# Optimization experiments

Hardware: AMD Instinct MI355X
Metric: run time of the kernel (lower is better)

Reference implementation:

```python
import jax, jax.numpy as jnp
import numpy as np

EPS = 1e-5

def conv2d(x, w, stride=1, padding=1, dilation=1):
    # x: [N, C, H, W], w: [O, I, kh, kw]
    return jax.lax.conv_general_dilated(
        x, w, (stride, stride), [(padding, padding), (padding, padding)],
        rhs_dilation=(dilation, dilation),
        dimension_numbers=('NCHW', 'OIHW', 'NCHW'))


def setup_inputs() -> dict:
    key = jax.random.key(0)
    ks = jax.random.split(key, 7)
    T, N, Cin, H, W = 16, 4, 64, 64, 64
    Cout = 64
    x = jax.random.normal(ks[0], (T, N, Cin, H, W), dtype=jnp.float32)
    gamma = jnp.ones((Cin,), jnp.float32)
    beta = jnp.zeros((Cin,), jnp.float32)
    conv1_w = jax.random.normal(ks[1], (3 * Cout, Cin, 3, 3), jnp.float32) * 0.02
    conv1_b = jax.random.normal(ks[2], (3 * Cout,), jnp.float32) * 0.02
    w_h2h = jax.random.normal(ks[3], (3 * Cout, Cout, 3, 3), jnp.float32) * 0.02
    w_c2h = jax.random.normal(ks[4], (3 * Cout, Cout, 3, 3), jnp.float32) * 0.02
    return {"x": x, "gamma": gamma, "beta": beta, "conv1_w": conv1_w,
            "conv1_b": conv1_b, "w_h2h": w_h2h, "w_c2h": w_c2h}


def reference(x, gamma, beta, conv1_w, conv1_b, w_h2h, w_c2h):
    T, N, Cin, H, W = x.shape
    Cout = w_h2h.shape[1]
    # time_to_batch: [T, N, C, H, W] -> [T*N, C, H, W]
    xb = x.reshape(T * N, Cin, H, W)
    # BatchNorm2d (training mode: biased batch stats over N*T, H, W)
    mean = jnp.mean(xb, axis=(0, 2, 3), keepdims=True)
    var = jnp.var(xb, axis=(0, 2, 3), keepdims=True)
    g = gamma.reshape(1, Cin, 1, 1)
    b = beta.reshape(1, Cin, 1, 1)
    bnx = (xb - mean) * jax.lax.rsqrt(var + EPS) * g + b
    # conv1: Cin -> 3*Cout
    y = conv2d(bnx, conv1_w, stride=1, padding=1) + conv1_b.reshape(1, -1, 1, 1)
    # batch_to_time: -> [T, N, 3*Cout, H, W]
    y = y.reshape(T, N, 3 * Cout, H, W)

    # ConvLSTMCell: zero init state is exact (h2h/c2h convs have no bias)
    h0 = jnp.zeros((N, Cout, H, W), y.dtype)
    c0 = jnp.zeros((N, Cout, H, W), y.dtype)

    def step(carry, yt):
        h, c = carry
        tmp = conv2d(c, w_c2h, padding=1) + conv2d(h, w_h2h, padding=1) + yt
        cc_f, cc_o, cc_g = jnp.split(tmp, 3, axis=1)
        f = jax.nn.sigmoid(cc_f)
        o = jax.nn.sigmoid(cc_o)
        gg = jnp.tanh(cc_g)
        c_new = f * c + (1.0 - f) * gg
        h_new = o * jnp.tanh(c_new)
        return (h_new, c_new), h_new

    _, hs = jax.lax.scan(step, (h0, c0), y)
    return hs  # [T, N, Cout, H, W]
```

## Files before the change

kernel.cpp:

```cpp
#include <hip/hip_runtime.h>

typedef unsigned short u16;
typedef unsigned int   u32;
typedef __attribute__((ext_vector_type(8))) short short8;
typedef __attribute__((ext_vector_type(4))) float f32x4;

typedef __attribute__((address_space(1))) const void GASV;
typedef __attribute__((address_space(3))) void LASV;

#define IMG_BYTES  557568
#define WS_SCALE   0
#define WS_SHIFT   256
#define WS_PART    512
#define WS_WA      8704
#define WS_BNXP    672256
#define WS_HC      (WS_BNXP + 64*IMG_BYTES)
#define WS_CSTATE  (WS_HC + 16*IMG_BYTES)

#define SM_IN(j)   ((j)*28512)
#define SM_WB(b)   (85536 + (b)*24576)
#define SMEM_TOT   159264

__device__ __forceinline__ u16 f2b(float f){
  u32 x = __float_as_uint(f);
  return (u16)((x + 0x7fffu + ((x>>16)&1u)) >> 16);
}
__device__ __forceinline__ float sigm(float x){ return 1.f/(1.f+__expf(-x)); }
__device__ __forceinline__ float tanh_(float x){
  float e = __expf(2.f*fabsf(x));
  float t = 1.f - 2.f/(e+1.f);
  return copysignf(t, x);
}

__global__ void k_wt(const float* __restrict__ c1, const float* __restrict__ c2h,
                     const float* __restrict__ h2h, u16* __restrict__ wA){
  int idx = blockIdx.x*256 + threadIdx.x;
  int e = idx & 7;
  int lane = (idx >> 3) & 63;
  int v = idx >> 9;
  int f = v % 12;  v /= 12;
  int cc = v & 1;  v >>= 1;
  int stage = v;
  int j = stage / 9, tap = stage % 9;
  int gate = f >> 2, og = f & 3;
  int och = gate*64 + og*16 + (lane & 15);
  int c = cc*32 + (lane >> 4)*8 + e;
  const float* src = (j==0) ? c1 : ((j==1) ? c2h : h2h);
  wA[idx] = f2b(src[(och*64 + c)*9 + tap]);
}

__global__ void k_bnsum(const float* __restrict__ x, float* __restrict__ part){
  int c = blockIdx.x & 63, g = blockIdx.x >> 6;
  int tid = threadIdx.x, w = tid >> 6, lane = tid & 63;
  float s = 0.f, s2 = 0.f;
  for (int im = 0; im < 4; ++im){
    const float* base = x + (((size_t)((g*4+im)*64 + c)) << 12);
    #pragma unroll
    for (int it = 0; it < 4; ++it){
      float4 v = *(const float4*)(base + (((it<<8) + tid) << 2));
      s  += v.x + v.y + v.z + v.w;
      s2 += v.x*v.x + v.y*v.y + v.z*v.z + v.w*v.w;
    }
  }
  #pragma unroll
  for (int off = 32; off > 0; off >>= 1){
    s  += __shfl_down(s,  off);
    s2 += __shfl_down(s2, off);
  }
  __shared__ float red[8];
  if (lane == 0){ red[w] = s; red[4+w] = s2; }
  __syncthreads();
  if (tid == 0){
    float S  = red[0]+red[1]+red[2]+red[3];
    float S2 = red[4]+red[5]+red[6]+red[7];
    part[(g<<7) + c] = S;
    part[(g<<7) + 64 + c] = S2;
  }
}

__global__ void k_bnfin(const float* __restrict__ part, const float* __restrict__ gamma,
                        const float* __restrict__ beta, float* __restrict__ scale,
                        float* __restrict__ shift){
  int c = threadIdx.x;
  float S = 0.f, S2 = 0.f;
  for (int g = 0; g < 16; ++g){ S += part[(g<<7)+c]; S2 += part[(g<<7)+64+c]; }
  const float inv = 1.f/262144.f;
  float mean = S*inv;
  float var  = S2*inv - mean*mean;
  float sc = gamma[c] * rsqrtf(var + 1e-5f);
  scale[c] = sc;
  shift[c] = beta[c] - mean*sc;
}

__global__ void k_bnx(const float* __restrict__ x, const float* __restrict__ scale,
                      const float* __restrict__ shift, char* __restrict__ bnxp){
  int img = blockIdx.x / 66, rp = blockIdx.x % 66;
  int tid = threadIdx.x;
  char* dstrow = bnxp + (size_t)img*IMG_BYTES + (size_t)rp*8448;
  const uint4 z = {0,0,0,0};
  if (rp == 0 || rp == 65){
    for (int i = tid; i < 528; i += 256) ((uint4*)dstrow)[i] = z;
    return;
  }
  if (tid < 16)
    *(uint4*)(dstrow + (tid>>3)*(65*128) + (tid&7)*16) = z;
  int r = rp - 1;
  int col = tid & 63, cq = tid >> 6;
  const float* xb = x + (((size_t)(img*64 + cq*16)) << 12) + (r<<6) + col;
  union { u16 u[16]; uint4 v[2]; } pk;
  #pragma unroll
  for (int i = 0; i < 16; ++i){
    int c = cq*16 + i;
    float vv = xb[((size_t)i) << 12];
    pk.u[i] = f2b(vv*scale[c] + shift[c]);
  }
  char* dst = dstrow + (size_t)(col + 1)*128 + cq*32;
  *(uint4*)dst = pk.v[0];
  *(uint4*)(dst+16) = pk.v[1];
}

#define STAGE_W(s, b) do {                                                      \
  const char* _gs = wA + (size_t)(s)*24576 + (w*3)*1024 + lane*16;              \
  char* _ls = smem + SM_WB(b) + (w*3)*1024;                                     \
  __builtin_amdgcn_global_load_lds((GASV*)(_gs),        (LASV*)(_ls),        16, 0, 0); \
  __builtin_amdgcn_global_load_lds((GASV*)(_gs + 1024), (LASV*)(_ls + 1024), 16, 0, 0); \
  __builtin_amdgcn_global_load_lds((GASV*)(_gs + 2048), (LASV*)(_ls + 2048), 16, 0, 0); \
} while(0)

__global__ __launch_bounds__(512, 1) void k_step(
    const char* __restrict__ bnxp,
    const char* __restrict__ cpad_s, const char* __restrict__ hpad_s,
    char* __restrict__ cpad_d, char* __restrict__ hpad_d,
    const char* __restrict__ wA, const float* __restrict__ b1,
    float* __restrict__ cstate, float* __restrict__ out, int t)
{
  extern __shared__ __align__(16) char smem[];
  const int tid = threadIdx.x;
  const int w = tid >> 6, lane = tid & 63;
  const int l15 = lane & 15, l4 = lane >> 4;
  const int og = w >> 1, ch = w & 1;
  const int n = blockIdx.x >> 6, row = blockIdx.x & 63;

  const char* gb0 = bnxp   + (size_t)(t*4+n)*IMG_BYTES + row*8448;
  const char* gb1 = cpad_s + (size_t)n*IMG_BYTES + row*8448;
  const char* gb2 = hpad_s + (size_t)n*IMG_BYTES + row*8448;

  f32x4 acc[3][2];
  #pragma unroll
  for (int a = 0; a < 3; ++a)
    #pragma unroll
    for (int b = 0; b < 2; ++b)
      acc[a][b] = (f32x4){0.f,0.f,0.f,0.f};

  STAGE_W(0, 0);
  STAGE_W(1, 1);

  #pragma unroll
  for (int j = 0; j < 3; ++j){
    const char* gbj = (j==0) ? gb0 : ((j==1) ? gb1 : gb2);
    char* dj = smem + SM_IN(j);
    #pragma unroll
    for (int rr = 0; rr < 3; ++rr){
      for (int i = tid; i < 528; i += 512)
        *(uint4*)(dj + rr*9504 + (i>>3)*144 + (i&7)*16) =
            *(const uint4*)(gbj + rr*8448 + i*16);
    }
  }
  __syncthreads();

  #pragma unroll
  for (int j = 0; j < 3; ++j){
    #pragma unroll
    for (int kh = 0; kh < 3; ++kh){
      #pragma unroll
      for (int kw = 0; kw < 3; ++kw){
        const int s = j*9 + kh*3 + kw;
        if (s < 25) STAGE_W(s+2, (s+2)%3);
        {
          const char* ab = smem + SM_WB(s%3) + og*1024 + lane*16;
          const char* ib = smem + SM_IN(j) + kh*9504 + ((ch<<5) + kw + l15)*144 + l4*16;
          #pragma unroll
          for (int cc = 0; cc < 2; ++cc){
            short8 af = *(const short8*)(ab + cc*12288);
            short8 ao = *(const short8*)(ab + cc*12288 + 4096);
            short8 ag = *(const short8*)(ab + cc*12288 + 8192);
            #pragma unroll
            for (int cf = 0; cf < 2; ++cf){
              short8 bf = *(const short8*)(ib + cc*64 + cf*2304);
              acc[0][cf] = __builtin_amdgcn_mfma_f32_16x16x32_bf16(af, bf, acc[0][cf], 0,0,0);
              acc[1][cf] = __builtin_amdgcn_mfma_f32_16x16x32_bf16(ao, bf, acc[1][cf], 0,0,0);
              acc[2][cf] = __builtin_amdgcn_mfma_f32_16x16x32_bf16(ag, bf, acc[2][cf], 0,0,0);
            }
          }
        }
        if (s < 26){
          if (s == 25) asm volatile("s_waitcnt vmcnt(0)" ::: "memory");
          else         asm volatile("s_waitcnt vmcnt(3)" ::: "memory");
          __builtin_amdgcn_s_barrier();
        }
      }
    }
  }

  const size_t cb = ((size_t)(n*64)) << 12;
  const size_t ob = ((size_t)((t*4+n)*64)) << 12;
  const int gc0 = (og << 4) + l4*4;
  char* hrow = hpad_d + (size_t)n*IMG_BYTES + (size_t)(row+1)*8448;
  char* crow = cpad_d + (size_t)n*IMG_BYTES + (size_t)(row+1)*8448;

  #pragma unroll
  for (int cf = 0; cf < 2; ++cf){
    const int col = (ch<<5) + (cf<<4) + l15;
    const int p = (row<<6) + col;
    union { u16 u[4]; uint2 v; } hp, cp2;
    #pragma unroll
    for (int reg = 0; reg < 4; ++reg){
      const int gc = gc0 + reg;
      float fv = acc[0][cf][reg] + b1[gc];
      float ov = acc[1][cf][reg] + b1[64+gc];
      float gv = acc[2][cf][reg] + b1[128+gc];
      float f  = sigm(fv);
      float og_ = sigm(ov);
      float g  = tanh_(gv);
      float* cptr = cstate + cb + (((size_t)gc)<<12) + p;
      float cprev = *cptr;
      float cn = f*cprev + (1.f-f)*g;
      float hn = og_ * tanh_(cn);
      *cptr = cn;
      out[ob + (((size_t)gc)<<12) + p] = hn;
      hp.u[reg]  = f2b(hn);
      cp2.u[reg] = f2b(cn);
    }
    *(uint2*)(hrow + (size_t)(col+1)*128 + gc0*2) = hp.v;
    *(uint2*)(crow + (size_t)(col+1)*128 + gc0*2) = cp2.v;
  }
}

extern "C" void kernel_launch(void* const* d_in, const int* in_sizes, int n_in,
                              void* d_out, int out_size, void* d_ws, size_t ws_size,
                              hipStream_t stream)
{
  (void)in_sizes; (void)n_in; (void)out_size; (void)ws_size;
  const float* x     = (const float*)d_in[0];
  const float* gamma = (const float*)d_in[1];
  const float* beta  = (const float*)d_in[2];
  const float* c1w   = (const float*)d_in[3];
  const float* c1b   = (const float*)d_in[4];
  const float* wh2h  = (const float*)d_in[5];
  const float* wc2h  = (const float*)d_in[6];
  char* ws  = (char*)d_ws;
  float* out = (float*)d_out;

  static int attr_done = 0;
  if (!attr_done){
    hipFuncSetAttribute(reinterpret_cast<const void*>(k_step),
                        hipFuncAttributeMaxDynamicSharedMemorySize, SMEM_TOT);
    attr_done = 1;
  }

  char* hpad0 = ws + WS_HC;
  char* cpad0 = ws + WS_HC + (size_t)4*IMG_BYTES;
  char* hpad1 = ws + WS_HC + (size_t)8*IMG_BYTES;
  char* cpad1 = ws + WS_HC + (size_t)12*IMG_BYTES;

  hipMemsetAsync(ws + WS_HC, 0, (size_t)16*IMG_BYTES, stream);
  hipMemsetAsync(ws + WS_CSTATE, 0, (size_t)4*64*4096*4, stream);

  k_wt<<<1296, 256, 0, stream>>>(c1w, wc2h, wh2h, (u16*)(ws + WS_WA));
  k_bnsum<<<1024, 256, 0, stream>>>(x, (float*)(ws + WS_PART));
  k_bnfin<<<1, 64, 0, stream>>>((const float*)(ws + WS_PART), gamma, beta,
                                (float*)(ws + WS_SCALE), (float*)(ws + WS_SHIFT));
  k_bnx<<<4224, 256, 0, stream>>>(x, (const float*)(ws + WS_SCALE),
                                  (const float*)(ws + WS_SHIFT), ws + WS_BNXP);
  for (int t = 0; t < 16; ++t){
    const char* cs = (t & 1) ? cpad1 : cpad0;
    const char* hs = (t & 1) ? hpad1 : hpad0;
    char* cd = (t & 1) ? cpad0 : cpad1;
    char* hd = (t & 1) ? hpad0 : hpad1;
    k_step<<<256, 512, SMEM_TOT, stream>>>(ws + WS_BNXP, cs, hs, cd, hd,
                                           ws + WS_WA, c1b,
                                           (float*)(ws + WS_CSTATE), out, t);
  }
}
```

Baseline: 389.8 us.

## Split output channels across two blocks and stream input images one at a time

Each step kernel now launches 512 blocks of 256 threads, and each block computes half of the output channel groups. The weight tensor is repacked to match this split. The three input images are no longer all staged up front: they are loaded into a single shared-memory buffer one after another, with a sync before each. Shared memory drops to about 64KB so two blocks can fit per CU. This aims to raise occupancy and spread work over more CUs, at the cost of loading each input row twice and adding barriers.

```diff
diff --git a/kernel.cpp b/kernel.cpp
--- a/kernel.cpp
+++ b/kernel.cpp
@@ -17,10 +17,6 @@
 #define WS_HC      (WS_BNXP + 64*IMG_BYTES)
 #define WS_CSTATE  (WS_HC + 16*IMG_BYTES)
 
-#define SM_IN(j)   ((j)*28512)
-#define SM_WB(b)   (85536 + (b)*24576)
-#define SMEM_TOT   159264
-
 __device__ __forceinline__ u16 f2b(float f){
   u32 x = __float_as_uint(f);
   return (u16)((x + 0x7fffu + ((x>>16)&1u)) >> 16);
@@ -38,12 +34,12 @@
   int e = idx & 7;
   int lane = (idx >> 3) & 63;
   int v = idx >> 9;
-  int f = v % 12;  v /= 12;
-  int cc = v & 1;  v >>= 1;
-  int stage = v;
+  int f2 = v % 12;  v /= 12;
+  int oh = v & 1;
+  int stage = v >> 1;
+  int cc = f2 / 6, gate = (f2 % 6) >> 1, og2 = f2 & 1;
   int j = stage / 9, tap = stage % 9;
-  int gate = f >> 2, og = f & 3;
-  int och = gate*64 + og*16 + (lane & 15);
+  int och = gate*64 + (oh*2 + og2)*16 + (lane & 15);
   int c = cc*32 + (lane >> 4)*8 + e;
   const float* src = (j==0) ? c1 : ((j==1) ? c2h : h2h);
   wA[idx] = f2b(src[(och*64 + c)*9 + tap]);
@@ -119,27 +115,39 @@
   *(uint4*)(dst+16) = pk.v[1];
 }
 
+#define SM_RING(b) (28512 + (b)*12288)
+
 #define STAGE_W(s, b) do {                                                      \
-  const char* _gs = wA + (size_t)(s)*24576 + (w*3)*1024 + lane*16;              \
-  char* _ls = smem + SM_WB(b) + (w*3)*1024;                                     \
+  const char* _gs = wA + ((size_t)((s)*2 + oh))*12288 + (w*3)*1024 + lane*16;   \
+  char* _ls = smem + SM_RING(b) + (w*3)*1024;                                   \
   __builtin_amdgcn_global_load_lds((GASV*)(_gs),        (LASV*)(_ls),        16, 0, 0); \
   __builtin_amdgcn_global_load_lds((GASV*)(_gs + 1024), (LASV*)(_ls + 1024), 16, 0, 0); \
   __builtin_amdgcn_global_load_lds((GASV*)(_gs + 2048), (LASV*)(_ls + 2048), 16, 0, 0); \
 } while(0)
 
-__global__ __launch_bounds__(512, 1) void k_step(
+#define WAIT3_BAR() do {                                                        \
+  asm volatile("s_waitcnt vmcnt(3)\n\ts_barrier" ::: "memory");                 \
+  __builtin_amdgcn_sched_barrier(0);                                            \
+} while(0)
+#define WAIT0_BAR() do {                                                        \
+  asm volatile("s_waitcnt vmcnt(0)\n\ts_barrier" ::: "memory");                 \
+  __builtin_amdgcn_sched_barrier(0);                                            \
+} while(0)
+
+__global__ __launch_bounds__(256, 2) void k_step(
     const char* __restrict__ bnxp,
     const char* __restrict__ cpad_s, const char* __restrict__ hpad_s,
     char* __restrict__ cpad_d, char* __restrict__ hpad_d,
     const char* __restrict__ wA, const float* __restrict__ b1,
     float* __restrict__ cstate, float* __restrict__ out, int t)
 {
-  extern __shared__ __align__(16) char smem[];
+  __shared__ __align__(16) char smem[65376];
   const int tid = threadIdx.x;
   const int w = tid >> 6, lane = tid & 63;
   const int l15 = lane & 15, l4 = lane >> 4;
-  const int og = w >> 1, ch = w & 1;
-  const int n = blockIdx.x >> 6, row = blockIdx.x & 63;
+  const int og2 = w >> 1, ch = w & 1;
+  const int bid = blockIdx.x;
+  const int oh = bid & 1, row = (bid >> 1) & 63, n = bid >> 7;
 
   const char* gb0 = bnxp   + (size_t)(t*4+n)*IMG_BYTES + row*8448;
   const char* gb1 = cpad_s + (size_t)n*IMG_BYTES + row*8448;
@@ -158,53 +166,45 @@
   #pragma unroll
   for (int j = 0; j < 3; ++j){
     const char* gbj = (j==0) ? gb0 : ((j==1) ? gb1 : gb2);
-    char* dj = smem + SM_IN(j);
-    #pragma unroll
-    for (int rr = 0; rr < 3; ++rr){
-      for (int i = tid; i < 528; i += 512)
-        *(uint4*)(dj + rr*9504 + (i>>3)*144 + (i&7)*16) =
-            *(const uint4*)(gbj + rr*8448 + i*16);
-    }
-  }
-  __syncthreads();
-
-  #pragma unroll
-  for (int j = 0; j < 3; ++j){
-    #pragma unroll
-    for (int kh = 0; kh < 3; ++kh){
-      #pragma unroll
-      for (int kw = 0; kw < 3; ++kw){
-        const int s = j*9 + kh*3 + kw;
-        if (s < 25) STAGE_W(s+2, (s+2)%3);
-        {
-          const char* ab = smem + SM_WB(s%3) + og*1024 + lane*16;
-          const char* ib = smem + SM_IN(j) + kh*9504 + ((ch<<5) + kw + l15)*144 + l4*16;
+    for (int i = tid; i < 1584; i += 256){
+      int rr = i / 528, iw = i % 528;
+      *(uint4*)(smem + rr*9504 + (iw>>3)*144 + (iw&7)*16) =
+          *(const uint4*)(gbj + rr*8448 + iw*16);
+    }
+    __syncthreads();
+
+    #pragma unroll
+    for (int tap = 0; tap < 9; ++tap){
+      const int s = j*9 + tap;
+      if (s < 25) STAGE_W(s+2, (s+2)%3);
+      {
+        const int kh = tap/3, kw = tap%3;
+        const char* ab0 = smem + SM_RING(s%3) + og2*1024 + lane*16;
+        const char* ib0 = smem + kh*9504 + ((ch<<5) + kw + l15)*144 + l4*16;
+        #pragma unroll
+        for (int cc = 0; cc < 2; ++cc){
+          short8 af = *(const short8*)(ab0 + cc*6144);
+          short8 ao = *(const short8*)(ab0 + cc*6144 + 2048);
+          short8 ag = *(const short8*)(ab0 + cc*6144 + 4096);
           #pragma unroll
-          for (int cc = 0; cc < 2; ++cc){
-            short8 af = *(const short8*)(ab + cc*12288);
-            short8 ao = *(const short8*)(ab + cc*12288 + 4096);
-            short8 ag = *(const short8*)(ab + cc*12288 + 8192);
-            #pragma unroll
-            for (int cf = 0; cf < 2; ++cf){
-              short8 bf = *(const short8*)(ib + cc*64 + cf*2304);
-              acc[0][cf] = __builtin_amdgcn_mfma_f32_16x16x32_bf16(af, bf, acc[0][cf], 0,0,0);
-              acc[1][cf] = __builtin_amdgcn_mfma_f32_16x16x32_bf16(ao, bf, acc[1][cf], 0,0,0);
-              acc[2][cf] = __builtin_amdgcn_mfma_f32_16x16x32_bf16(ag, bf, acc[2][cf], 0,0,0);
-            }
+          for (int cf = 0; cf < 2; ++cf){
+            short8 bf = *(const short8*)(ib0 + cc*64 + cf*2304);
+            acc[0][cf] = __builtin_amdgcn_mfma_f32_16x16x32_bf16(af, bf, acc[0][cf], 0,0,0);
+            acc[1][cf] = __builtin_amdgcn_mfma_f32_16x16x32_bf16(ao, bf, acc[1][cf], 0,0,0);
+            acc[2][cf] = __builtin_amdgcn_mfma_f32_16x16x32_bf16(ag, bf, acc[2][cf], 0,0,0);
           }
         }
-        if (s < 26){
-          if (s == 25) asm volatile("s_waitcnt vmcnt(0)" ::: "memory");
-          else         asm volatile("s_waitcnt vmcnt(3)" ::: "memory");
-          __builtin_amdgcn_s_barrier();
-        }
+      }
+      if (s < 26){
+        if (s == 25) WAIT0_BAR();
+        else         WAIT3_BAR();
       }
     }
   }
 
   const size_t cb = ((size_t)(n*64)) << 12;
   const size_t ob = ((size_t)((t*4+n)*64)) << 12;
-  const int gc0 = (og << 4) + l4*4;
+  const int gc0 = ((oh<<1) + og2)*16 + l4*4;
   char* hrow = hpad_d + (size_t)n*IMG_BYTES + (size_t)(row+1)*8448;
   char* crow = cpad_d + (size_t)n*IMG_BYTES + (size_t)(row+1)*8448;
 
@@ -251,13 +251,6 @@
   char* ws  = (char*)d_ws;
   float* out = (float*)d_out;
 
-  static int attr_done = 0;
-  if (!attr_done){
-    hipFuncSetAttribute(reinterpret_cast<const void*>(k_step),
-                        hipFuncAttributeMaxDynamicSharedMemorySize, SMEM_TOT);
-    attr_done = 1;
-  }
-
   char* hpad0 = ws + WS_HC;
   char* cpad0 = ws + WS_HC + (size_t)4*IMG_BYTES;
   char* hpad1 = ws + WS_HC + (size_t)8*IMG_BYTES;
@@ -277,8 +270,8 @@
     const char* hs = (t & 1) ? hpad1 : hpad0;
     char* cd = (t & 1) ? cpad0 : cpad1;
     char* hd = (t & 1) ? hpad0 : hpad1;
-    k_step<<<256, 512, SMEM_TOT, stream>>>(ws + WS_BNXP, cs, hs, cd, hd,
-                                           ws + WS_WA, c1b,
-                                           (float*)(ws + WS_CSTATE), out, t);
-  }
-}
+    k_step<<<512, 256, 0, stream>>>(ws + WS_BNXP, cs, hs, cd, hd,
+                                    ws + WS_WA, c1b,
+                                    (float*)(ws + WS_CSTATE), out, t);
+  }
+}
```

New measurement: 391.6 us. Within noise of the previous version (+0.5%).
